# Kernel optimization log

Measured on AMD Instinct MI355X. Metric: run time of the kernel, lower is better.

Reference implementation:

```python
import jax, jax.numpy as jnp
import numpy as np

N_WIRES = 4
DIM = 2 ** N_WIRES  # 16-dim statevector


def _zsigns():
    # PauliZ sign per basis state; wire 0 is the most-significant bit
    idx = np.arange(DIM)
    signs = np.stack([1 - 2 * ((idx >> (N_WIRES - 1 - w)) & 1) for w in range(N_WIRES)], 0)
    return jnp.asarray(signs, jnp.float32)  # [4, 16]

ZSIGNS = _zsigns()


def _apply_rx(state, ang, w):
    # state: [B, 16] complex64, ang: [B] rotation angle on wire w
    B = state.shape[0]
    s = state.reshape(B, 2 ** w, 2, 2 ** (N_WIRES - 1 - w))
    c = jnp.cos(ang * 0.5)[:, None, None]
    sn = jnp.sin(ang * 0.5)[:, None, None]
    s0, s1 = s[:, :, 0, :], s[:, :, 1, :]
    o0 = c * s0 - 1j * sn * s1
    o1 = -1j * sn * s0 + c * s1
    return jnp.stack([o0, o1], axis=2).reshape(B, DIM)


def _cnot(state, c, t):
    # flip target bit t where control bit c == 1
    B = state.shape[0]
    s = state.reshape((B,) + (2,) * N_WIRES)
    ca, ta = c + 1, t + 1  # +1 for batch axis
    s0 = jnp.take(s, 0, axis=ca)
    s1 = jnp.take(s, 1, axis=ca)
    t_ax = ta - 1 if ta > ca else ta  # target axis shifts after control axis removed
    s1 = jnp.flip(s1, axis=t_ax)     # size-2 flip == Pauli-X
    return jnp.stack([s0, s1], axis=ca).reshape(B, DIM)


def _qgate(v, theta):
    # v: [B, 4] encoder angles, theta: [4] trainable RX angles (RX angles add)
    B = v.shape[0]
    ang = v + theta[None, :]
    state = jnp.zeros((B, DIM), jnp.complex64).at[:, 0].set(1.0)
    for w in range(N_WIRES):
        state = _apply_rx(state, ang[:, w], w)
    for w in range(N_WIRES):
        state = _cnot(state, w, (w + 1) % N_WIRES)
    probs = jnp.real(state * jnp.conj(state))  # [B, 16]
    return probs @ ZSIGNS.T                    # [B, 4] <Z> per wire


def setup_inputs() -> dict:
    key = jax.random.key(0)
    ks = jax.random.split(key, 16)
    B, S, V, E, H, T = 256, 128, 32000, 256, 4, 32
    d_in = E + H
    sc = 1.0 / np.sqrt(d_in)
    inp = {
        'x': jax.random.randint(ks[0], (B, S), 0, V),
        'embedding': jax.random.normal(ks[1], (V, E), jnp.float32) * 0.02,
        'Wf': jax.random.normal(ks[2], (H, d_in), jnp.float32) * sc,
        'bf': jnp.zeros((H,), jnp.float32),
        'Wi': jax.random.normal(ks[3], (H, d_in), jnp.float32) * sc,
        'bi': jnp.zeros((H,), jnp.float32),
        'Wu': jax.random.normal(ks[4], (H, d_in), jnp.float32) * sc,
        'bu': jnp.zeros((H,), jnp.float32),
        'Wo': jax.random.normal(ks[5], (H, d_in), jnp.float32) * sc,
        'bo': jnp.zeros((H,), jnp.float32),
        'theta_f': jax.random.uniform(ks[6], (H,), jnp.float32, 0.0, 2 * np.pi),
        'theta_i': jax.random.uniform(ks[7], (H,), jnp.float32, 0.0, 2 * np.pi),
        'theta_u': jax.random.uniform(ks[8], (H,), jnp.float32, 0.0, 2 * np.pi),
        'theta_o': jax.random.uniform(ks[9], (H,), jnp.float32, 0.0, 2 * np.pi),
        'Wc': jax.random.normal(ks[10], (T, H), jnp.float32) * 0.5,
        'bc': jnp.zeros((T,), jnp.float32),
    }
    return inp


def reference(x, embedding, Wf, bf, Wi, bi, Wu, bu, Wo, bo,
              theta_f, theta_i, theta_u, theta_o, Wc, bc):
    emb = embedding[x]  # [B, S, E]
    B, S, E = emb.shape
    H = Wf.shape[0]

    def step(carry, xt):
        hx, cx = carry
        comb = jnp.concatenate([xt, hx], axis=1)  # [B, E+H]
        f = jax.nn.sigmoid(_qgate(comb @ Wf.T + bf, theta_f))
        i = jax.nn.sigmoid(_qgate(comb @ Wi.T + bi, theta_i))
        g = jnp.tanh(_qgate(comb @ Wu.T + bu, theta_u))
        o = jax.nn.sigmoid(_qgate(comb @ Wo.T + bo, theta_o))
        cx = f * cx + i * g
        hx = o * jnp.tanh(cx)
        return (hx, cx), hx

    h0 = jnp.zeros((B, H), emb.dtype)
    (_, _), hs = jax.lax.scan(step, (h0, h0), jnp.swapaxes(emb, 0, 1))
    lstm_out = jnp.swapaxes(hs, 0, 1)        # [B, S, H]
    logits = lstm_out @ Wc.T + bc            # [B, S, T]
    return jax.nn.log_softmax(logits, axis=-1)
```

## Files before the change

### kernel.cpp

```cpp
#include <hip/hip_runtime.h>
#include <math.h>

constexpr int NB = 256;
constexpr int NS = 128;
constexpr int NE = 256;
constexpr int DIN = 260;

__device__ __forceinline__ float rcp_fast(float x) {
#if __has_builtin(__builtin_amdgcn_rcpf)
    return __builtin_amdgcn_rcpf(x);
#else
    return 1.0f / x;
#endif
}

#if __has_builtin(__builtin_amdgcn_mov_dpp)
#define DPP_XOR1(x) __int_as_float(__builtin_amdgcn_mov_dpp(__float_as_int(x), 0xB1, 0xF, 0xF, true))
#define DPP_XOR2(x) __int_as_float(__builtin_amdgcn_mov_dpp(__float_as_int(x), 0x4E, 0xF, 0xF, true))
#define DPP_XOR3(x) __int_as_float(__builtin_amdgcn_mov_dpp(__float_as_int(x), 0x1B, 0xF, 0xF, true))
#else
#define DPP_XOR1(x) __shfl_xor((x), 1, 64)
#define DPP_XOR2(x) __shfl_xor((x), 2, 64)
#define DPP_XOR3(x) __shfl_xor((x), 3, 64)
#endif

__device__ __forceinline__ float tanh_cf(float y) {
    float w = y * y;
    float num = y * fmaf(fmaf(21.0f, w, 1260.0f), w, 10395.0f);
    float den = fmaf(fmaf(w + 210.0f, w, 4725.0f), w, 10395.0f);
    return num * rcp_fast(den);
}

__device__ __forceinline__ float sel4f(float v0, float v1, float v2, float v3,
                                       bool bit0, bool bit1) {
    float lo = bit0 ? v1 : v0;
    float hi = bit0 ? v3 : v2;
    return bit1 ? hi : lo;
}

__device__ __forceinline__ void gload_lds16(const void* gsrc, void* ldst) {
    __builtin_amdgcn_global_load_lds(
        (const __attribute__((address_space(1))) void*)gsrc,
        (__attribute__((address_space(3))) void*)ldst, 16, 0, 0);
}

__global__ __launch_bounds__(256) void k_embed(
    const int* __restrict__ x, const float* __restrict__ emb,
    const float* __restrict__ Wf, const float* __restrict__ bf,
    const float* __restrict__ Wi, const float* __restrict__ bi,
    const float* __restrict__ Wu, const float* __restrict__ bu,
    const float* __restrict__ Wo, const float* __restrict__ bo,
    const float* __restrict__ thf, const float* __restrict__ thi,
    const float* __restrict__ thu, const float* __restrict__ tho,
    float* __restrict__ xpart)
{
    const int lane = threadIdx.x & 63;
    const int wave_id = blockIdx.x * 4 + (threadIdx.x >> 6);

    float4 Wreg[16];
    #pragma unroll
    for (int j = 0; j < 16; ++j) {
        const float* Wgp = (j < 8) ? ((j < 4) ? Wf : Wi) : ((j < 12) ? Wu : Wo);
        Wreg[j] = *(const float4*)(Wgp + (j & 3) * DIN + lane * 4);
    }
    float biasv;
    {
        int j = lane & 15, jj = j & 3;
        const float* bp = (j < 8) ? ((j < 4) ? bf : bi) : ((j < 12) ? bu : bo);
        const float* tp = (j < 8) ? ((j < 4) ? thf : thi) : ((j < 12) ? thu : tho);
        biasv = bp[jj] + tp[jj];
    }

    const bool p0 = (lane & 1) != 0, p1 = (lane & 2) != 0,
               p2 = (lane & 4) != 0, p3 = (lane & 8) != 0;

    const int row0 = wave_id * 16;

#define LDE(I) (*(const float4*)(emb + \
    (size_t)x[((row0 + (I)) & 255) * NS + ((row0 + (I)) >> 8)] * NE + lane * 4))

#define PROC(I, EV) do {                                                     \
    float acc[16];                                                           \
    _Pragma("unroll")                                                        \
    for (int j = 0; j < 16; ++j) {                                           \
        float4 wv = Wreg[j];                                                 \
        acc[j] = fmaf((EV).x, wv.x, fmaf((EV).y, wv.y,                       \
                  fmaf((EV).z, wv.z, (EV).w * wv.w)));                       \
    }                                                                        \
    float t8[8];                                                             \
    _Pragma("unroll")                                                        \
    for (int i2 = 0; i2 < 8; ++i2) {                                         \
        float keep = p0 ? acc[2 * i2 + 1] : acc[2 * i2];                     \
        float send = p0 ? acc[2 * i2] : acc[2 * i2 + 1];                     \
        t8[i2] = keep + __shfl_xor(send, 1, 64);                             \
    }                                                                        \
    float t4[4];                                                             \
    _Pragma("unroll")                                                        \
    for (int i2 = 0; i2 < 4; ++i2) {                                         \
        float keep = p1 ? t8[2 * i2 + 1] : t8[2 * i2];                       \
        float send = p1 ? t8[2 * i2] : t8[2 * i2 + 1];                       \
        t4[i2] = keep + __shfl_xor(send, 2, 64);                             \
    }                                                                        \
    float t2[2];                                                             \
    _Pragma("unroll")                                                        \
    for (int i2 = 0; i2 < 2; ++i2) {                                         \
        float keep = p2 ? t4[2 * i2 + 1] : t4[2 * i2];                       \
        float send = p2 ? t4[2 * i2] : t4[2 * i2 + 1];                       \
        t2[i2] = keep + __shfl_xor(send, 4, 64);                             \
    }                                                                        \
    float keep = p3 ? t2[1] : t2[0];                                         \
    float send = p3 ? t2[0] : t2[1];                                         \
    float t1 = keep + __shfl_xor(send, 8, 64);                               \
    t1 += __shfl_xor(t1, 16, 64);                                            \
    t1 += __shfl_xor(t1, 32, 64);                                            \
    if (lane < 16)                                                           \
        xpart[(size_t)(row0 + (I)) * 16 + lane] = t1 + biasv;                \
} while (0)

    float4 ev0 = LDE(0), ev1 = LDE(1), ev2 = LDE(2), ev3 = LDE(3);
    PROC(0,  ev0); ev0 = LDE(4);
    PROC(1,  ev1); ev1 = LDE(5);
    PROC(2,  ev2); ev2 = LDE(6);
    PROC(3,  ev3); ev3 = LDE(7);
    PROC(4,  ev0); ev0 = LDE(8);
    PROC(5,  ev1); ev1 = LDE(9);
    PROC(6,  ev2); ev2 = LDE(10);
    PROC(7,  ev3); ev3 = LDE(11);
    PROC(8,  ev0); ev0 = LDE(12);
    PROC(9,  ev1); ev1 = LDE(13);
    PROC(10, ev2); ev2 = LDE(14);
    PROC(11, ev3); ev3 = LDE(15);
    PROC(12, ev0);
    PROC(13, ev1);
    PROC(14, ev2);
    PROC(15, ev3);
#undef PROC
#undef LDE
}

__global__ __launch_bounds__(64) void k_recur(
    const float* __restrict__ Wf, const float* __restrict__ Wi,
    const float* __restrict__ Wu, const float* __restrict__ Wo,
    const float* __restrict__ xpart, float* __restrict__ hs)
{
    __shared__ float4 xlds[2][16][64];
    __shared__ float  hlds[128][64];

    const int lane = threadIdx.x;
    const int g = lane & 3;
    const int b0 = blockIdx.x * 16;

    const float* Wg = (g == 0) ? Wf : ((g == 1) ? Wi : ((g == 2) ? Wu : Wo));
    float Wp[4][4];
    #pragma unroll
    for (int j2 = 0; j2 < 4; ++j2)
        #pragma unroll
        for (int k = 0; k < 4; ++k)
            Wp[j2][k] = Wg[j2 * DIN + 256 + (g ^ k)];

    const bool bb0 = (g & 1) != 0, bb1 = (g & 2) != 0;
    const float scl = (g == 2) ? 1.0f : 0.5f;
    const float mlt = (g == 2) ? 1.0f : 0.5f;
    const float bas = (g == 2) ? 0.0f : 0.5f;
    const float s2 = scl * scl;
    const float D0 = mlt * 0.999416f * scl;
    const float D1 = mlt * -0.326958f * scl * s2;
    const float D2 = mlt * 0.111796f * scl * s2 * s2;
    const float D3 = mlt * -0.022660f * scl * s2 * s2 * s2;

    float c = 0.0f;
    float hr0 = 0.f, hr1 = 0.f, hr2 = 0.f, hr3 = 0.f;

    const char* xblk = (const char*)xpart + (size_t)b0 * 64 + (size_t)lane * 16;

    #pragma unroll
    for (int i = 0; i < 16; ++i)
        gload_lds16(xblk + (size_t)i * 16384, &xlds[0][i][0]);
    #pragma unroll
    for (int i = 0; i < 16; ++i)
        gload_lds16(xblk + (size_t)(16 + i) * 16384, &xlds[1][i][0]);
    asm volatile("s_waitcnt vmcnt(16)" ::: "memory");

#define GACT(Q) ({ float wq_ = (Q) * (Q);                                     \
    float pp_ = fmaf(fmaf(fmaf(D3, wq_, D2), wq_, D1), wq_, D0);              \
    fmaf((Q), pp_, bas); })

#define QS(I) do {                                                            \
    float4 xc = xlds[bsel][I][lane];                                          \
    float m0 = fmaf(Wp[0][2], hr2, Wp[0][3] * hr3);                           \
    float v0 = fmaf(Wp[0][1], hr1, m0);                                       \
    float u0 = fmaf(Wp[0][0], hr0, xc.x);                                     \
    float a0 = u0 + v0;                                                       \
    float m1 = fmaf(Wp[1][2], hr2, Wp[1][3] * hr3);                           \
    float v1 = fmaf(Wp[1][1], hr1, m1);                                       \
    float u1 = fmaf(Wp[1][0], hr0, xc.y);                                     \
    float a1 = u1 + v1;                                                       \
    float m2 = fmaf(Wp[2][2], hr2, Wp[2][3] * hr3);                           \
    float v2 = fmaf(Wp[2][1], hr1, m2);                                       \
    float u2 = fmaf(Wp[2][0], hr0, xc.z);                                     \
    float a2 = u2 + v2;                                                       \
    float m3 = fmaf(Wp[3][2], hr2, Wp[3][3] * hr3);                           \
    float v3 = fmaf(Wp[3][1], hr1, m3);                                       \
    float u3 = fmaf(Wp[3][0], hr0, xc.w);                                     \
    float a3 = u3 + v3;                                                       \
    float c0_ = __cosf(a0), c1_ = __cosf(a1), c2_ = __cosf(a2), c3_ = __cosf(a3); \
    float tt = c2_ * c3_;                                                     \
    float q1 = c0_ * c1_;                                                     \
    float q0 = c1_ * tt;                                                      \
    float q2 = q1 * c2_;                                                      \
    float q3 = q1 * tt;                                                       \
    float A0 = GACT(q0);                                                      \
    float A1 = GACT(q1);                                                      \
    float A2 = GACT(q2);                                                      \
    float A3 = GACT(q3);                                                      \
    float r1 = DPP_XOR1(sel4f(A0, A1, A2, A3, !bb0,  bb1));                   \
    float r2 = DPP_XOR2(sel4f(A0, A1, A2, A3,  bb0, !bb1));                   \
    float r3 = DPP_XOR3(sel4f(A0, A1, A2, A3, !bb0, !bb1));                   \
    float r0 = sel4f(A0, A1, A2, A3, bb0, bb1);                               \
    float fv = sel4f(r0, r1, r2, r3,  bb0,  bb1);                             \
    float iv = sel4f(r0, r1, r2, r3, !bb0,  bb1);                             \
    float uv = sel4f(r0, r1, r2, r3,  bb0, !bb1);                             \
    float ov = sel4f(r0, r1, r2, r3, !bb0, !bb1);                             \
    c = fmaf(fv, c, iv * uv);                                                 \
    float hn = ov * tanh_cf(c);                                               \
    hlds[(cc << 4) + I][lane] = hn;                                           \
    hr0 = hn;                                                                 \
    hr1 = DPP_XOR1(hn);                                                       \
    hr2 = DPP_XOR2(hn);                                                       \
    hr3 = DPP_XOR3(hn);                                                       \
} while (0)

    for (int cc = 0; cc < 8; ++cc) {
        const int bsel = cc & 1;
        QS(0);  QS(1);  QS(2);  QS(3);
        QS(4);  QS(5);  QS(6);  QS(7);
        QS(8);  QS(9);  QS(10); QS(11);
        QS(12); QS(13); QS(14); QS(15);
        if (cc < 6) {
            #pragma unroll
            for (int i = 0; i < 16; ++i)
                gload_lds16(xblk + (size_t)((cc + 2) * 16 + i) * 16384,
                            &xlds[bsel][i][0]);
            asm volatile("s_waitcnt vmcnt(16)" ::: "memory");
        } else if (cc == 6) {
            asm volatile("s_waitcnt vmcnt(0)" ::: "memory");
        }
    }
#undef QS
#undef GACT

    #pragma unroll 4
    for (int j = 0; j < 32; ++j) {
        int sp = j * 4 + (lane >> 4);
        float4 v = *(const float4*)&hlds[sp][(lane & 15) * 4];
        *(float4*)(hs + (size_t)sp * 1024 + (size_t)b0 * 4 + (lane & 15) * 4) = v;
    }
}

__global__ __launch_bounds__(256) void k_out(
    const float* __restrict__ hs, const float* __restrict__ Wc,
    const float* __restrict__ bc, float* __restrict__ out)
{
    int gtid = blockIdx.x * 256 + threadIdx.x;
    int r = gtid >> 3;
    int lr = gtid & 7;
    if (r >= NB * NS) return;
    int b = r >> 7, s = r & 127;
    float4 h = *(const float4*)(hs + ((size_t)s * NB + b) * 4);
    float l[4];
    #pragma unroll
    for (int k = 0; k < 4; ++k) {
        int t = lr * 4 + k;
        float4 w = *(const float4*)(Wc + t * 4);
        l[k] = bc[t] + w.x * h.x + w.y * h.y + w.z * h.z + w.w * h.w;
    }
    float m = fmaxf(fmaxf(l[0], l[1]), fmaxf(l[2], l[3]));
    #pragma unroll
    for (int msk = 1; msk < 8; msk <<= 1)
        m = fmaxf(m, __shfl_xor(m, msk, 64));
    float sum = 0.f;
    #pragma unroll
    for (int k = 0; k < 4; ++k)
        sum += __expf(l[k] - m);
    #pragma unroll
    for (int msk = 1; msk < 8; msk <<= 1)
        sum += __shfl_xor(sum, msk, 64);
    float lse = __logf(sum);
    float4 o;
    o.x = l[0] - m - lse;
    o.y = l[1] - m - lse;
    o.z = l[2] - m - lse;
    o.w = l[3] - m - lse;
    *(float4*)(out + (size_t)r * 32 + lr * 4) = o;
}

extern "C" void kernel_launch(void* const* d_in, const int* in_sizes, int n_in,
                              void* d_out, int out_size, void* d_ws, size_t ws_size,
                              hipStream_t stream) {
    const int*   x   = (const int*)d_in[0];
    const float* emb = (const float*)d_in[1];
    const float* Wf  = (const float*)d_in[2];
    const float* bf  = (const float*)d_in[3];
    const float* Wi  = (const float*)d_in[4];
    const float* bi  = (const float*)d_in[5];
    const float* Wu  = (const float*)d_in[6];
    const float* bu  = (const float*)d_in[7];
    const float* Wo  = (const float*)d_in[8];
    const float* bo  = (const float*)d_in[9];
    const float* thf = (const float*)d_in[10];
    const float* thi = (const float*)d_in[11];
    const float* thu = (const float*)d_in[12];
    const float* tho = (const float*)d_in[13];
    const float* Wc  = (const float*)d_in[14];
    const float* bc  = (const float*)d_in[15];
    float* out = (float*)d_out;

    float* xpart = (float*)d_ws;
    float* hs    = xpart + (size_t)NS * NB * 16;

    k_embed<<<512, 256, 0, stream>>>(x, emb, Wf, bf, Wi, bi, Wu, bu, Wo, bo,
                                     thf, thi, thu, tho, xpart);
    k_recur<<<16, 64, 0, stream>>>(Wf, Wi, Wu, Wo, xpart, hs);
    k_out<<<1024, 256, 0, stream>>>(hs, Wc, bc, out);
}
```

Measured before the change: 47.87 us.

## Prescale angles by 1/2π, use packed FMA and raw v_cos in recurrence

Folds the 1/(2π) factor into the input projection weights, bias and recurrent weights so the cosine can run as v_fract plus v_cos_f32 directly on revolutions. This skips the range reduction that __cosf performs. The recurrent matvec and the gate polynomial are rewritten with 2-wide float vectors so the compiler can emit packed FMA (v_pk_fma_f32), shortening the serial per-step critical path. The embed kernel also widens its load prefetch from 4 to 6 rows in flight, which adds register pressure.

```diff
diff --git a/kernel.cpp b/kernel.cpp
--- a/kernel.cpp
+++ b/kernel.cpp
@@ -5,6 +5,11 @@
 constexpr int NS = 128;
 constexpr int NE = 256;
 constexpr int DIN = 260;
+
+typedef float f2 __attribute__((ext_vector_type(2)));
+#define fma2(A, B, C) __builtin_elementwise_fma((A), (B), (C))
+
+constexpr float INV2PI = 0.15915494309189535f;
 
 __device__ __forceinline__ float rcp_fast(float x) {
 #if __has_builtin(__builtin_amdgcn_rcpf)
@@ -12,6 +17,13 @@
 #else
     return 1.0f / x;
 #endif
+}
+
+__device__ __forceinline__ float cos_rev(float x) {
+    float f, r;
+    asm("v_fract_f32 %0, %1" : "=v"(f) : "v"(x));
+    asm("v_cos_f32 %0, %1" : "=v"(r) : "v"(f));
+    return r;
 }
 
 #if __has_builtin(__builtin_amdgcn_mov_dpp)
@@ -61,14 +73,15 @@
     #pragma unroll
     for (int j = 0; j < 16; ++j) {
         const float* Wgp = (j < 8) ? ((j < 4) ? Wf : Wi) : ((j < 12) ? Wu : Wo);
-        Wreg[j] = *(const float4*)(Wgp + (j & 3) * DIN + lane * 4);
+        float4 w = *(const float4*)(Wgp + (j & 3) * DIN + lane * 4);
+        Wreg[j] = make_float4(w.x * INV2PI, w.y * INV2PI, w.z * INV2PI, w.w * INV2PI);
     }
     float biasv;
     {
         int j = lane & 15, jj = j & 3;
         const float* bp = (j < 8) ? ((j < 4) ? bf : bi) : ((j < 12) ? bu : bo);
         const float* tp = (j < 8) ? ((j < 4) ? thf : thi) : ((j < 12) ? thu : tho);
-        biasv = bp[jj] + tp[jj];
+        biasv = (bp[jj] + tp[jj]) * INV2PI;
     }
 
     const bool p0 = (lane & 1) != 0, p1 = (lane & 2) != 0,
@@ -117,19 +130,20 @@
         xpart[(size_t)(row0 + (I)) * 16 + lane] = t1 + biasv;                \
 } while (0)
 
-    float4 ev0 = LDE(0), ev1 = LDE(1), ev2 = LDE(2), ev3 = LDE(3);
-    PROC(0,  ev0); ev0 = LDE(4);
-    PROC(1,  ev1); ev1 = LDE(5);
-    PROC(2,  ev2); ev2 = LDE(6);
-    PROC(3,  ev3); ev3 = LDE(7);
-    PROC(4,  ev0); ev0 = LDE(8);
-    PROC(5,  ev1); ev1 = LDE(9);
-    PROC(6,  ev2); ev2 = LDE(10);
-    PROC(7,  ev3); ev3 = LDE(11);
-    PROC(8,  ev0); ev0 = LDE(12);
-    PROC(9,  ev1); ev1 = LDE(13);
-    PROC(10, ev2); ev2 = LDE(14);
-    PROC(11, ev3); ev3 = LDE(15);
+    float4 ev0 = LDE(0), ev1 = LDE(1), ev2 = LDE(2),
+           ev3 = LDE(3), ev4 = LDE(4), ev5 = LDE(5);
+    PROC(0,  ev0); ev0 = LDE(6);
+    PROC(1,  ev1); ev1 = LDE(7);
+    PROC(2,  ev2); ev2 = LDE(8);
+    PROC(3,  ev3); ev3 = LDE(9);
+    PROC(4,  ev4); ev4 = LDE(10);
+    PROC(5,  ev5); ev5 = LDE(11);
+    PROC(6,  ev0); ev0 = LDE(12);
+    PROC(7,  ev1); ev1 = LDE(13);
+    PROC(8,  ev2); ev2 = LDE(14);
+    PROC(9,  ev3); ev3 = LDE(15);
+    PROC(10, ev4);
+    PROC(11, ev5);
     PROC(12, ev0);
     PROC(13, ev1);
     PROC(14, ev2);
@@ -151,22 +165,26 @@
     const int b0 = blockIdx.x * 16;
 
     const float* Wg = (g == 0) ? Wf : ((g == 1) ? Wi : ((g == 2) ? Wu : Wo));
-    float Wp[4][4];
-    #pragma unroll
-    for (int j2 = 0; j2 < 4; ++j2)
-        #pragma unroll
-        for (int k = 0; k < 4; ++k)
-            Wp[j2][k] = Wg[j2 * DIN + 256 + (g ^ k)];
+    f2 W01[4], W23[4];
+    #pragma unroll
+    for (int k = 0; k < 4; ++k) {
+        W01[k] = f2{Wg[0 * DIN + 256 + (g ^ k)] * INV2PI,
+                    Wg[1 * DIN + 256 + (g ^ k)] * INV2PI};
+        W23[k] = f2{Wg[2 * DIN + 256 + (g ^ k)] * INV2PI,
+                    Wg[3 * DIN + 256 + (g ^ k)] * INV2PI};
+    }
 
     const bool bb0 = (g & 1) != 0, bb1 = (g & 2) != 0;
     const float scl = (g == 2) ? 1.0f : 0.5f;
     const float mlt = (g == 2) ? 1.0f : 0.5f;
     const float bas = (g == 2) ? 0.0f : 0.5f;
     const float s2 = scl * scl;
-    const float D0 = mlt * 0.999416f * scl;
-    const float D1 = mlt * -0.326958f * scl * s2;
-    const float D2 = mlt * 0.111796f * scl * s2 * s2;
-    const float D3 = mlt * -0.022660f * scl * s2 * s2 * s2;
+    const float e0 = mlt * 0.999416f * scl;
+    const float e1 = mlt * -0.326958f * scl * s2;
+    const float e2 = mlt * 0.111796f * scl * s2 * s2;
+    const float e3 = mlt * -0.022660f * scl * s2 * s2 * s2;
+    const f2 D0d = {e0, e0}, D1d = {e1, e1}, D2d = {e2, e2}, D3d = {e3, e3};
+    const f2 basd = {bas, bas};
 
     float c = 0.0f;
     float hr0 = 0.f, hr1 = 0.f, hr2 = 0.f, hr3 = 0.f;
@@ -181,38 +199,30 @@
         gload_lds16(xblk + (size_t)(16 + i) * 16384, &xlds[1][i][0]);
     asm volatile("s_waitcnt vmcnt(16)" ::: "memory");
 
-#define GACT(Q) ({ float wq_ = (Q) * (Q);                                     \
-    float pp_ = fmaf(fmaf(fmaf(D3, wq_, D2), wq_, D1), wq_, D0);              \
-    fmaf((Q), pp_, bas); })
-
 #define QS(I) do {                                                            \
     float4 xc = xlds[bsel][I][lane];                                          \
-    float m0 = fmaf(Wp[0][2], hr2, Wp[0][3] * hr3);                           \
-    float v0 = fmaf(Wp[0][1], hr1, m0);                                       \
-    float u0 = fmaf(Wp[0][0], hr0, xc.x);                                     \
-    float a0 = u0 + v0;                                                       \
-    float m1 = fmaf(Wp[1][2], hr2, Wp[1][3] * hr3);                           \
-    float v1 = fmaf(Wp[1][1], hr1, m1);                                       \
-    float u1 = fmaf(Wp[1][0], hr0, xc.y);                                     \
-    float a1 = u1 + v1;                                                       \
-    float m2 = fmaf(Wp[2][2], hr2, Wp[2][3] * hr3);                           \
-    float v2 = fmaf(Wp[2][1], hr1, m2);                                       \
-    float u2 = fmaf(Wp[2][0], hr0, xc.z);                                     \
-    float a2 = u2 + v2;                                                       \
-    float m3 = fmaf(Wp[3][2], hr2, Wp[3][3] * hr3);                           \
-    float v3 = fmaf(Wp[3][1], hr1, m3);                                       \
-    float u3 = fmaf(Wp[3][0], hr0, xc.w);                                     \
-    float a3 = u3 + v3;                                                       \
-    float c0_ = __cosf(a0), c1_ = __cosf(a1), c2_ = __cosf(a2), c3_ = __cosf(a3); \
+    f2 x01 = {xc.x, xc.y}, x23 = {xc.z, xc.w};                                \
+    f2 h0d = {hr0, hr0}, h1d = {hr1, hr1}, h2d = {hr2, hr2}, h3d = {hr3, hr3};\
+    f2 a01 = fma2(W01[0], h0d, x01);                                          \
+    a01 = fma2(W01[1], h1d, a01);                                             \
+    a01 = fma2(W01[2], h2d, a01);                                             \
+    a01 = fma2(W01[3], h3d, a01);                                             \
+    f2 a23 = fma2(W23[0], h0d, x23);                                          \
+    a23 = fma2(W23[1], h1d, a23);                                             \
+    a23 = fma2(W23[2], h2d, a23);                                             \
+    a23 = fma2(W23[3], h3d, a23);                                             \
+    float c0_ = cos_rev(a01.x), c1_ = cos_rev(a01.y);                         \
+    float c2_ = cos_rev(a23.x), c3_ = cos_rev(a23.y);                         \
     float tt = c2_ * c3_;                                                     \
     float q1 = c0_ * c1_;                                                     \
-    float q0 = c1_ * tt;                                                      \
-    float q2 = q1 * c2_;                                                      \
-    float q3 = q1 * tt;                                                       \
-    float A0 = GACT(q0);                                                      \
-    float A1 = GACT(q1);                                                      \
-    float A2 = GACT(q2);                                                      \
-    float A3 = GACT(q3);                                                      \
+    f2 q01 = {c1_ * tt, q1};                                                  \
+    f2 q23 = {q1 * c2_, q1 * tt};                                             \
+    f2 w01 = q01 * q01, w23 = q23 * q23;                                      \
+    f2 p01 = fma2(fma2(fma2(D3d, w01, D2d), w01, D1d), w01, D0d);             \
+    f2 p23 = fma2(fma2(fma2(D3d, w23, D2d), w23, D1d), w23, D0d);             \
+    f2 A01 = fma2(q01, p01, basd);                                            \
+    f2 A23 = fma2(q23, p23, basd);                                            \
+    float A0 = A01.x, A1 = A01.y, A2 = A23.x, A3 = A23.y;                     \
     float r1 = DPP_XOR1(sel4f(A0, A1, A2, A3, !bb0,  bb1));                   \
     float r2 = DPP_XOR2(sel4f(A0, A1, A2, A3,  bb0, !bb1));                   \
     float r3 = DPP_XOR3(sel4f(A0, A1, A2, A3, !bb0, !bb1));                   \
@@ -247,7 +257,6 @@
         }
     }
 #undef QS
-#undef GACT
 
     #pragma unroll 4
     for (int j = 0; j < 32; ++j) {
```

Measured after the change: 45.04 us. -5.9%, faster.
